# Optimization experiments

Measured on AMD Instinct MI355X. Metric: run time of the kernel, lower is better.

Reference implementation:

```python
import jax, jax.numpy as jnp
import numpy as np

N_SAMPLES = 32768; WINDOW = 512; STEP = 256; N_FRAMES = 128
N_COEFFS = 257; N_ATOMS = 32; MODEL_DIM = 128
DILATIONS = (1, 3, 9, 27, 81, 243, 1)


def _conv1d(x, w, b=None, dilation=1, padding=0):
    o = jax.lax.conv_general_dilated(x, w, (1,), [(padding, padding)],
                                     rhs_dilation=(dilation,),
                                     dimension_numbers=('NCH', 'OIH', 'NCH'))
    return o if b is None else o + b[None, :, None]


def _leaky(x):
    return jnp.where(x >= 0, x, 0.2 * x)


def _lin_stack(x, ws, bs, ow, ob):
    # LinearOutputStack: hidden linears with leaky relu, final linear
    for i in range(ws.shape[0]):
        x = _leaky(x @ ws[i].T + bs[i])
    return x @ ow.T + ob


def _conv_up(z, lw, lb, cw, cb, fw, fb_):
    x = (z @ lw.T + lb).reshape(-1, MODEL_DIM, 8)
    for i in range(cw.shape[0]):
        x = jnp.repeat(x, 2, axis=-1)
        x = _leaky(_conv1d(x, cw[i], cb[i], padding=1))
    return _conv1d(x, fw, fb_, padding=1)


def _lin_upsample(x, out_len):
    # F.upsample(mode='linear', align_corners=False)
    L = x.shape[-1]
    src = jnp.clip((jnp.arange(out_len) + 0.5) * (L / out_len) - 0.5, 0.0, L - 1)
    i0 = jnp.floor(src).astype(jnp.int32)
    i1 = jnp.minimum(i0 + 1, L - 1)
    t = (src - i0).astype(x.dtype)
    return x[..., i0] * (1 - t) + x[..., i1] * t


def _generate_event(envelope, transfer, impulse_tf, impulse_noise):
    # envelope [N,1,S], transfer [N,257,2,128], impulse_tf [N,257,2]
    tf = jax.lax.complex(transfer[:, :, 0, :], transfer[:, :, 1, :])  # [N,257,128]
    itf = jax.lax.complex(impulse_tf[..., 0], impulse_tf[..., 1])     # [N,257]
    spec = jnp.fft.rfft(impulse_noise, norm='ortho') * itf
    impulse = jnp.fft.irfft(spec, n=WINDOW, norm='ortho')             # [N,512]
    env = jnp.pad(envelope[:, 0, :], ((0, 0), (0, STEP)))             # pad last frame
    win_idx = (jnp.arange(N_FRAMES) * STEP)[:, None] + jnp.arange(WINDOW)  # [128,512]
    env_frames = env[:, win_idx]                                      # [N,128,512]
    ham = (0.54 - 0.46 * jnp.cos(2 * jnp.pi * jnp.arange(WINDOW) / WINDOW)).astype(envelope.dtype)

    def step(carry, inp):
        env_f, tf_f = inp                      # [N,512], [N,257]
        nxt = impulse * env_f + carry
        s = jnp.fft.rfft(nxt, norm='ortho') * tf_f
        out = jnp.fft.irfft(s, n=WINDOW, norm='ortho') * ham
        return out, out

    _, frames = jax.lax.scan(step, jnp.zeros_like(impulse),
                             (env_frames.transpose(1, 0, 2), tf.transpose(2, 0, 1)))
    frames = frames.transpose(1, 0, 2)         # [N,128,512]
    buf = jnp.zeros((frames.shape[0], N_FRAMES * STEP + STEP), frames.dtype)
    buf = buf.at[:, win_idx].add(frames)       # overlap-add, hop 256
    return buf[:, :N_SAMPLES]


def reference(x, fb_w,
              db_scale_w, db_scale_b, db_gate_w, db_gate_b,
              db_out_w, db_out_b, db_next_w, db_next_b,
              env_lin_w, env_lin_b, env_conv_w, env_conv_b, env_fin_w, env_fin_b,
              tf_lin_w, tf_lin_b, tf_conv_w, tf_conv_b, tf_fin_w, tf_fin_b,
              imp_w, imp_b, imp_out_w, imp_out_b,
              room_w, room_b, room_out_w, room_out_b,
              mix_w, mix_b, mix_out_w, mix_out_b,
              rooms, impulse_noise):
    B = x.shape[0]
    # FilterBank: conv over raw audio, same length
    n = jax.lax.conv_general_dilated(x, fb_w, (1,), [(256, 255)],
                                     dimension_numbers=('NCH', 'OIH', 'NCH'))  # [B,128,S]
    acc = jnp.zeros_like(n)
    for i, d in enumerate(DILATIONS):
        skip = n
        s = _conv1d(n, db_scale_w[i], db_scale_b[i], dilation=d, padding=d)
        g = _conv1d(n, db_gate_w[i], db_gate_b[i], dilation=d, padding=d)
        h = jnp.tanh(s) * jax.nn.sigmoid(g)
        acc = acc + jnp.einsum('oc,bct->bot', db_out_w[i], h) + db_out_b[i][None, :, None]
        n = jnp.einsum('oc,bct->bot', db_next_w[i], h) + db_next_b[i][None, :, None] + skip
    xf = acc                                                   # [B,128,S]
    norms = jnp.linalg.norm(xf, axis=1)                        # [B,S]
    values, indices = jax.lax.top_k(norms, N_ATOMS)            # [B,32]
    latents = jnp.take_along_axis(xf, indices[:, None, :], axis=2)  # [B,128,32]
    latents = latents.transpose(0, 2, 1).reshape(B * N_ATOMS, MODEL_DIM)
    # EventGenerator
    env = _conv_up(latents, env_lin_w, env_lin_b, env_conv_w, env_conv_b, env_fin_w, env_fin_b) ** 2
    env = _lin_upsample(env, N_SAMPLES)                        # [N,1,S]
    transfer = _conv_up(latents, tf_lin_w, tf_lin_b, tf_conv_w, tf_conv_b, tf_fin_w, tf_fin_b)
    transfer = transfer.reshape(-1, N_COEFFS, 2, N_FRAMES)
    impulse_tf = _lin_stack(latents, imp_w, imp_b, imp_out_w, imp_out_b).reshape(-1, N_COEFFS, 2)
    atoms = _generate_event(env, transfer, impulse_tf, impulse_noise).reshape(B, N_ATOMS, N_SAMPLES)
    # scatter-add atoms at topk offsets into 2*S buffer
    pos = indices[:, :, None] + jnp.arange(N_SAMPLES)[None, None, :]   # [B,32,S]
    weighted = atoms * values[:, :, None]

    def scat(pos_b, w_b):
        return jnp.zeros(2 * N_SAMPLES, w_b.dtype).at[pos_b.reshape(-1)].add(w_b.reshape(-1))

    final = jax.vmap(scat)(pos, weighted)[:, None, :N_SAMPLES]         # [B,1,S]
    # reverb mix
    agg = jnp.max(xf, axis=-1)                                         # [B,128]
    r = _lin_stack(agg, room_w, room_b, room_out_w, room_out_b)        # [B,n_rooms]
    m = _lin_stack(agg, mix_w, mix_b, mix_out_w, mix_out_b).reshape(-1, 1, 1)
    ir = jax.nn.softmax(r, axis=-1) @ rooms                            # [B,S]
    fs = jnp.fft.rfft(final[:, 0, :], n=2 * N_SAMPLES)
    irs = jnp.fft.rfft(ir, n=2 * N_SAMPLES)
    wet = jnp.fft.irfft(fs * irs, n=2 * N_SAMPLES)[:, None, :N_SAMPLES]
    return m * wet + final * (1 - m)


def setup_inputs() -> dict:
    key = jax.random.key(0)
    ks = iter(jax.random.split(key, 64))

    def w(*shape, s=0.05):
        return jax.random.normal(next(ks), shape, dtype=jnp.float32) * s

    return {
        'x': jax.random.normal(next(ks), (4, 1, N_SAMPLES), dtype=jnp.float32),
        'fb_w': w(128, 1, 512),
        'db_scale_w': w(7, 128, 128, 3), 'db_scale_b': w(7, 128),
        'db_gate_w': w(7, 128, 128, 3), 'db_gate_b': w(7, 128),
        'db_out_w': w(7, 128, 128), 'db_out_b': w(7, 128),
        'db_next_w': w(7, 128, 128), 'db_next_b': w(7, 128),
        'env_lin_w': w(1024, 128), 'env_lin_b': w(1024),
        'env_conv_w': w(4, 128, 128, 3), 'env_conv_b': w(4, 128),
        'env_fin_w': w(1, 128, 3), 'env_fin_b': w(1),
        'tf_lin_w': w(1024, 128), 'tf_lin_b': w(1024),
        'tf_conv_w': w(4, 128, 128, 3), 'tf_conv_b': w(4, 128),
        'tf_fin_w': w(514, 128, 3), 'tf_fin_b': w(514),
        'imp_w': w(3, 128, 128), 'imp_b': w(3, 128),
        'imp_out_w': w(514, 128), 'imp_out_b': w(514),
        'room_w': w(3, 128, 128), 'room_b': w(3, 128),
        'room_out_w': w(8, 128), 'room_out_b': w(8),
        'mix_w': w(3, 128, 128), 'mix_b': w(3, 128),
        'mix_out_w': w(1, 128), 'mix_out_b': w(1),
        'rooms': w(8, N_SAMPLES, s=0.1),
        'impulse_noise': jax.random.uniform(next(ks), (1, WINDOW), minval=-1.0, maxval=1.0, dtype=jnp.float32),
    }
```

## Files before the change

### kernel.cpp

```cpp
#include <hip/hip_runtime.h>
#include <math.h>

#define NS 32768

static __device__ __forceinline__ float leakyf(float x){ return x >= 0.f ? x : 0.2f*x; }

__global__ void k_wtrans(const float* __restrict__ ws, const float* __restrict__ wg, float* __restrict__ wT)
{
    int idx = blockIdx.x*256 + threadIdx.x;
    const int total = 7*2*3*128*128;
    if (idx >= total) return;
    int o  = idx & 127;
    int cc = (idx >> 7) & 127;
    int j  = (idx >> 14) % 3;
    int sg = (idx / 49152) & 1;
    int l  = idx / 98304;
    const float* src = sg ? wg : ws;
    wT[idx] = src[((l*128 + o)*128 + cc)*3 + j];
}

__global__ void k_wtrans2(const float* __restrict__ wo, const float* __restrict__ wn,
                          float* __restrict__ woT, float* __restrict__ wnT)
{
    int idx = blockIdx.x*256 + threadIdx.x;
    if (idx >= 7*128*128) return;
    int o = idx & 127;
    int c = (idx >> 7) & 127;
    int l = idx >> 14;
    woT[idx] = wo[(l*128 + o)*128 + c];
    wnT[idx] = wn[(l*128 + o)*128 + c];
}

__global__ void k_wtrans_up(const float* __restrict__ ecw, const float* __restrict__ tcw,
                            const float* __restrict__ tfw, float* __restrict__ wtu, float* __restrict__ wtf)
{
    int idx = blockIdx.x*256 + threadIdx.x;
    if (idx < 393216) {
        int o = idx & 127;
        int j = (idx >> 7) % 3;
        int c = (idx / 384) & 127;
        int ml = idx / 49152;
        const float* src = (ml < 4 ? ecw : tcw) + (ml & 3)*49152;
        wtu[idx] = src[(o*128 + c)*3 + j];
    }
    if (idx < 208896) {
        int ct = idx % 544;
        int j = (idx / 544) % 3;
        int c = idx / 1632;
        wtf[idx] = (ct < 514) ? tfw[(ct*128 + c)*3 + j] : 0.f;
    }
}

__global__ __launch_bounds__(512) void k_front(const float* __restrict__ x, const float* __restrict__ fbw,
                                               float* __restrict__ n0)
{
    int b = blockIdx.y;
    int t0 = blockIdx.x * 64;
    int tid = threadIdx.x;
    int t = tid & 63, og = tid >> 6;
    __shared__ float xs[576];
    __shared__ float4 wl[2048];
    for (int i = tid; i < 575; i += 512) {
        int p = t0 + i - 256;
        xs[i] = ((unsigned)p < NS) ? x[b*NS + p] : 0.f;
    }
    float s[16];
    #pragma unroll
    for (int i = 0; i < 16; ++i) s[i] = 0.f;
    for (int kc = 0; kc < 8; ++kc) {
        __syncthreads();
        for (int i = tid; i < 2048; i += 512) {
            int c = i >> 4, k4 = i & 15;
            wl[i] = *(const float4*)(fbw + c*512 + kc*64 + k4*4);
        }
        __syncthreads();
        for (int k4 = 0; k4 < 16; ++k4) {
            int base = t + kc*64 + k4*4;
            float xv0 = xs[base+0], xv1 = xs[base+1], xv2 = xs[base+2], xv3 = xs[base+3];
            #pragma unroll
            for (int i = 0; i < 16; ++i) {
                float4 w = wl[(og*16 + i)*16 + k4];
                s[i] += w.x*xv0 + w.y*xv1 + w.z*xv2 + w.w*xv3;
            }
        }
    }
    #pragma unroll
    for (int i = 0; i < 16; ++i)
        n0[(size_t)(b*128 + og*16 + i)*NS + t0 + t] = s[i];
}

__global__ __launch_bounds__(512) void k_layer(const float* __restrict__ nin, float* __restrict__ nout,
        float* __restrict__ acc, const float* __restrict__ wTl,
        const float* __restrict__ bs, const float* __restrict__ bg,
        const float* __restrict__ woTl, const float* __restrict__ bo,
        const float* __restrict__ wnTl, const float* __restrict__ bn,
        int d, int first)
{
    __shared__ float pool[20480];
    int b = blockIdx.y;
    int t0 = blockIdx.x * 128;
    int tid = threadIdx.x;
    int l = tid & 31, og = tid >> 5;
    int o0 = og * 8;
    int t4 = l * 4;
    const float* nb = nin + (size_t)b*128*NS;
    const float4* wq = (const float4*)wTl;

    int sci = tid >> 5;
    int st4 = (tid & 31) * 4;
    int wsgA = 0,              wccA = (tid >> 5) & 15,        wo4A = tid & 31;
    int wsgB = (tid+512) >> 9, wccB = ((tid+512) >> 5) & 15,  wo4B = (tid+512) & 31;

    float4 sreg, wr0, wr1;
    {
        int p = t0 + st4 - d;
        const float* bp = nb + (size_t)sci*NS;
        float v0 = ((unsigned)(p+0) < NS) ? bp[p+0] : 0.f;
        float v1 = ((unsigned)(p+1) < NS) ? bp[p+1] : 0.f;
        float v2 = ((unsigned)(p+2) < NS) ? bp[p+2] : 0.f;
        float v3 = ((unsigned)(p+3) < NS) ? bp[p+3] : 0.f;
        sreg = make_float4(v0,v1,v2,v3);
        wr0 = wq[((wsgA*3 + 0)*128 + wccA)*32 + wo4A];
        wr1 = wq[((wsgB*3 + 0)*128 + wccB)*32 + wo4B];
    }

    float sA[8], sB[8], sC[8], sD[8], gA[8], gB[8], gC[8], gD[8];
    #pragma unroll
    for (int i = 0; i < 8; ++i) {
        float bv = bs[o0+i], gv = bg[o0+i];
        sA[i]=bv; sB[i]=bv; sC[i]=bv; sD[i]=bv;
        gA[i]=gv; gB[i]=gv; gC[i]=gv; gD[i]=gv;
    }

    #pragma unroll 1
    for (int cnt = 0; cnt < 24; ++cnt) {
        int cur = cnt & 1;
        ((float4*)(pool + cur*2048))[tid] = sreg;
        {
            float4* wb = (float4*)(pool + 4096 + cur*4096);
            wb[tid] = wr0; wb[tid + 512] = wr1;
        }
        if (cnt < 23) {
            int nxt = cnt + 1;
            int jn = nxt >> 3, cbn = nxt & 7;
            int p = t0 + st4 + (jn-1)*d;
            const float* bp = nb + (size_t)(cbn*16 + sci)*NS;
            float v0 = ((unsigned)(p+0) < NS) ? bp[p+0] : 0.f;
            float v1 = ((unsigned)(p+1) < NS) ? bp[p+1] : 0.f;
            float v2 = ((unsigned)(p+2) < NS) ? bp[p+2] : 0.f;
            float v3 = ((unsigned)(p+3) < NS) ? bp[p+3] : 0.f;
            sreg = make_float4(v0,v1,v2,v3);
            wr0 = wq[((wsgA*3 + jn)*128 + cbn*16 + wccA)*32 + wo4A];
            wr1 = wq[((wsgB*3 + jn)*128 + cbn*16 + wccB)*32 + wo4B];
        }
        __syncthreads();
        const float* sb = pool + cur*2048;
        const float4* wS4 = (const float4*)(pool + 4096 + cur*4096);
        const float4* wG4 = wS4 + 512;
        for (int ccx = 0; ccx < 16; ++ccx) {
            float4 nv = *(const float4*)(sb + ccx*128 + t4);
            #pragma unroll
            for (int i4 = 0; i4 < 2; ++i4) {
                float4 wsv = wS4[ccx*32 + og*2 + i4];
                float4 wgv = wG4[ccx*32 + og*2 + i4];
                int ib = i4*4;
#define ST1(CMP, OO) \
                sA[OO] += nv.x*wsv.CMP; sB[OO] += nv.y*wsv.CMP; sC[OO] += nv.z*wsv.CMP; sD[OO] += nv.w*wsv.CMP; \
                gA[OO] += nv.x*wgv.CMP; gB[OO] += nv.y*wgv.CMP; gC[OO] += nv.z*wgv.CMP; gD[OO] += nv.w*wgv.CMP;
                ST1(x, ib+0) ST1(y, ib+1) ST1(z, ib+2) ST1(w, ib+3)
#undef ST1
            }
        }
    }

    __syncthreads();
    #pragma unroll
    for (int i = 0; i < 8; ++i) {
        float h0 = tanhf(sA[i]) * (1.f/(1.f + __expf(-gA[i])));
        float h1 = tanhf(sB[i]) * (1.f/(1.f + __expf(-gB[i])));
        float h2 = tanhf(sC[i]) * (1.f/(1.f + __expf(-gC[i])));
        float h3 = tanhf(sD[i]) * (1.f/(1.f + __expf(-gD[i])));
        *(float4*)(pool + (o0+i)*128 + t4) = make_float4(h0,h1,h2,h3);
    }

    int aarm = tid >> 8, arest = tid & 255;
    int accx = arest >> 5, ao4 = arest & 31;
    float4 w2r;
    {
        const float4* src = (const float4*)(aarm ? wnTl : woTl);
        w2r = src[(0*8 + accx)*32 + ao4];
    }

    float aA[8], aB[8], aC[8], aD[8], nA[8], nB[8], nC[8], nD[8];
    #pragma unroll
    for (int i = 0; i < 8; ++i) { aA[i]=0.f;aB[i]=0.f;aC[i]=0.f;aD[i]=0.f;nA[i]=0.f;nB[i]=0.f;nC[i]=0.f;nD[i]=0.f; }

    #pragma unroll 1
    for (int cb2 = 0; cb2 < 16; ++cb2) {
        int cur = cb2 & 1;
        ((float4*)(pool + 16384 + cur*2048))[tid] = w2r;
        if (cb2 < 15) {
            const float4* src = (const float4*)(aarm ? wnTl : woTl);
            w2r = src[((cb2+1)*8 + accx)*32 + ao4];
        }
        __syncthreads();
        const float4* w2S = (const float4*)(pool + 16384 + cur*2048);
        const float4* w2N = w2S + 256;
        for (int ccx = 0; ccx < 8; ++ccx) {
            float4 hv = *(const float4*)(pool + (cb2*8 + ccx)*128 + t4);
            #pragma unroll
            for (int i4 = 0; i4 < 2; ++i4) {
                float4 wov = w2S[ccx*32 + og*2 + i4];
                float4 wnv = w2N[ccx*32 + og*2 + i4];
                int ib = i4*4;
#define ST2(CMP, OO) \
                aA[OO] += hv.x*wov.CMP; aB[OO] += hv.y*wov.CMP; aC[OO] += hv.z*wov.CMP; aD[OO] += hv.w*wov.CMP; \
                nA[OO] += hv.x*wnv.CMP; nB[OO] += hv.y*wnv.CMP; nC[OO] += hv.z*wnv.CMP; nD[OO] += hv.w*wnv.CMP;
                ST2(x, ib+0) ST2(y, ib+1) ST2(z, ib+2) ST2(w, ib+3)
#undef ST2
            }
        }
    }

    #pragma unroll
    for (int i = 0; i < 8; ++i) {
        int o = o0 + i;
        float bov = bo[o], bnv = bn[o];
        size_t gi = (size_t)(b*128 + o)*NS + t0 + t4;
        float4 av = first ? make_float4(0.f,0.f,0.f,0.f) : *(const float4*)(acc + gi);
        float4 nf = *(const float4*)(nin + gi);
        *(float4*)(acc + gi)  = make_float4(av.x + aA[i] + bov, av.y + aB[i] + bov,
                                            av.z + aC[i] + bov, av.w + aD[i] + bov);
        *(float4*)(nout + gi) = make_float4(nA[i] + bnv + nf.x, nB[i] + bnv + nf.y,
                                            nC[i] + bnv + nf.z, nD[i] + bnv + nf.w);
    }
}

__global__ void k_norms(const float* __restrict__ xf, float* __restrict__ norms)
{
    int b = blockIdx.y;
    int t = blockIdx.x*256 + threadIdx.x;
    float a = 0.f;
    for (int c = 0; c < 128; ++c) {
        float v = xf[(size_t)(b*128 + c)*NS + t];
        a += v*v;
    }
    norms[b*NS + t] = a;
}

__global__ __launch_bounds__(1024) void k_topk(float* __restrict__ norms, float* __restrict__ topv, int* __restrict__ topi)
{
    int b = blockIdx.x;
    int tid = threadIdx.x;
    __shared__ float rv[1024];
    __shared__ int   ri[1024];
    for (int it = 0; it < 32; ++it) {
        float best = -2.f; int bi = 0;
        for (int k = tid; k < NS; k += 1024) {
            float v = norms[b*NS + k];
            if (v > best) { best = v; bi = k; }
        }
        rv[tid] = best; ri[tid] = bi;
        __syncthreads();
        for (int off = 512; off > 0; off >>= 1) {
            if (tid < off) {
                float ov = rv[tid+off]; int oi = ri[tid+off];
                if (ov > rv[tid] || (ov == rv[tid] && oi < ri[tid])) { rv[tid] = ov; ri[tid] = oi; }
            }
            __syncthreads();
        }
        if (tid == 0) {
            topv[b*32 + it] = sqrtf(rv[0]);
            topi[b*32 + it] = ri[0];
            norms[b*NS + ri[0]] = -1.f;
        }
        __syncthreads();
    }
}

__global__ void k_latents(const float* __restrict__ xf, const int* __restrict__ topi, float* __restrict__ lat)
{
    int ev = blockIdx.x; int c = threadIdx.x;
    int b = ev >> 5;
    int idx = topi[ev];
    lat[ev*128 + c] = xf[(size_t)(b*128 + c)*NS + idx];
}

__global__ void k_aggmax(const float* __restrict__ xf, float* __restrict__ agg)
{
    int rc = blockIdx.x;
    int tid = threadIdx.x;
    __shared__ float red[256];
    float m = -3.4e38f;
    const float* row = xf + (size_t)rc*NS;
    for (int t = tid; t < NS; t += 256) m = fmaxf(m, row[t]);
    red[tid] = m; __syncthreads();
    for (int off = 128; off > 0; off >>= 1) {
        if (tid < off) red[tid] = fmaxf(red[tid], red[tid+off]);
        __syncthreads();
    }
    if (tid == 0) agg[rc] = red[0];
}

template<int L2, int NPASS>
__device__ __forceinline__ void up_layerS(const float* __restrict__ wbase, const float* __restrict__ bias,
                                          const float* __restrict__ inb, float* __restrict__ outb,
                                          float* __restrict__ wst, int tid)
{
    constexpr int Lin = L2/2;
    constexpr int OGC = 512/L2;
    constexpr int OR  = 128/NPASS;
    constexpr int NO  = OR/OGC;
    constexpr int LOG = (L2==16)?4:(L2==32)?5:(L2==64)?6:7;
    int p  = tid & (L2-1);
    int og = tid >> LOG;
    int o0 = og*NO;
    #pragma unroll 1
    for (int pass = 0; pass < NPASS; ++pass) {
        int obase = pass*OR;
        float acc[NO];
        #pragma unroll
        for (int k = 0; k < NO; ++k) acc[k] = 0.f;
        #pragma unroll 1
        for (int cc0 = 0; cc0 < 128; cc0 += 16) {
            __syncthreads();
            for (int k = tid; k < 16*3*OR; k += 512) {
                int ci = k / (3*OR); int rem = k - ci*(3*OR);
                int j = rem / OR; int oo = rem - j*OR;
                wst[k] = wbase[(cc0+ci)*384 + j*128 + obase + oo];
            }
            __syncthreads();
            #pragma unroll 1
            for (int ci = 0; ci < 16; ++ci) {
                int c = cc0 + ci;
                float xv[3];
                #pragma unroll
                for (int j = 0; j < 3; ++j) {
                    int iu = p + j - 1;
                    xv[j] = ((unsigned)iu < (unsigned)L2) ? inb[c*Lin + (iu>>1)] : 0.f;
                }
                #pragma unroll
                for (int j = 0; j < 3; ++j) {
                    const float4* w4 = (const float4*)(wst + ci*3*OR + j*OR + o0);
                    #pragma unroll
                    for (int q = 0; q < NO/4; ++q) {
                        float4 w = w4[q];
                        acc[q*4+0] += xv[j]*w.x; acc[q*4+1] += xv[j]*w.y;
                        acc[q*4+2] += xv[j]*w.z; acc[q*4+3] += xv[j]*w.w;
                    }
                }
            }
        }
        #pragma unroll
        for (int k = 0; k < NO; ++k)
            outb[(obase + o0 + k)*L2 + p] = leakyf(acc[k] + bias[obase + o0 + k]);
    }
}

__global__ __launch_bounds__(512) void k_convup3(const float* __restrict__ lat,
    const float* __restrict__ elw, const float* __restrict__ elb, const float* __restrict__ ecb,
    const float* __restrict__ efw, const float* __restrict__ efb,
    const float* __restrict__ tlw, const float* __restrict__ tlb, const float* __restrict__ tcb,
    const float* __restrict__ tfb, const float* __restrict__ wtu, const float* __restrict__ wtf,
    float* __restrict__ envsq, float* __restrict__ tfT)
{
    __shared__ float pool[35008];
    float* latv = pool;
    float* bufA = pool + 128;
    float* bufB = pool + 4288;
    float* bufC = pool + 12480;
    float* wst  = pool + 28864;
    int ev = blockIdx.x;
    int m  = blockIdx.y;
    int tid = threadIdx.x;
    const float* lw = m ? tlw : elw;
    const float* lb = m ? tlb : elb;
    const float* cb = m ? tcb : ecb;
    const float* wu = wtu + m*4*49152;
    if (tid < 128) latv[tid] = lat[ev*128 + tid];
    __syncthreads();
    for (int jj = tid; jj < 1024; jj += 512) {
        float a = lb[jj];
        const float4* w4 = (const float4*)(lw + jj*128);
        #pragma unroll 8
        for (int q = 0; q < 32; ++q) {
            float4 w = w4[q];
            a += w.x*latv[q*4] + w.y*latv[q*4+1] + w.z*latv[q*4+2] + w.w*latv[q*4+3];
        }
        bufA[(jj>>3)*8 + (jj&7)] = a;
    }
    up_layerS<16,1>(wu,        cb,     bufA, bufB, wst, tid);
    up_layerS<32,1>(wu+49152,  cb+128, bufB, bufA, wst, tid);
    up_layerS<64,2>(wu+98304,  cb+256, bufA, bufB, wst, tid);
    up_layerS<128,4>(wu+147456,cb+384, bufB, bufC, wst, tid);
    __syncthreads();
    int p = tid & 127, g = tid >> 7;
    if (m == 0) {
        float s = 0.f;
        #pragma unroll 1
        for (int c = g*32; c < g*32+32; ++c) {
            #pragma unroll
            for (int j = 0; j < 3; ++j) {
                int iu = p + j - 1;
                float xv = ((unsigned)iu < 128u) ? bufC[c*128 + iu] : 0.f;
                s += efw[c*3+j]*xv;
            }
        }
        wst[g*128 + p] = s;
        __syncthreads();
        if (g == 0) {
            float a = wst[p] + wst[128+p] + wst[256+p] + wst[384+p] + efb[0];
            envsq[ev*128 + p] = a*a;
        }
    } else {
        float* trb = bufA;
        #pragma unroll 1
        for (int ctb = 0; ctb < 17; ++ctb) {
            int ct0 = ctb*32;
            float acc[8];
            #pragma unroll
            for (int i = 0; i < 8; ++i) acc[i] = 0.f;
            #pragma unroll 1
            for (int cc0 = 0; cc0 < 128; cc0 += 16) {
                __syncthreads();
                for (int k = tid; k < 1536; k += 512) {
                    int ci = k / 96, rem = k - ci*96;
                    int j = rem >> 5, ctl = rem & 31;
                    wst[k] = wtf[(cc0+ci)*1632 + j*544 + ct0 + ctl];
                }
                __syncthreads();
                #pragma unroll 1
                for (int ci = 0; ci < 16; ++ci) {
                    int c = cc0 + ci;
                    float xv[3];
                    #pragma unroll
                    for (int j = 0; j < 3; ++j) {
                        int iu = p + j - 1;
                        xv[j] = ((unsigned)iu < 128u) ? bufC[c*128 + iu] : 0.f;
                    }
                    #pragma unroll
                    for (int j = 0; j < 3; ++j) {
                        const float4* w4 = (const float4*)(wst + ci*96 + j*32 + g*8);
                        #pragma unroll
                        for (int q = 0; q < 2; ++q) {
                            float4 w = w4[q];
                            acc[q*4+0] += xv[j]*w.x; acc[q*4+1] += xv[j]*w.y;
                            acc[q*4+2] += xv[j]*w.z; acc[q*4+3] += xv[j]*w.w;
                        }
                    }
                }
            }
            __syncthreads();
            #pragma unroll
            for (int i = 0; i < 8; ++i) trb[(g*8 + i)*129 + p] = acc[i];
            __syncthreads();
            int ctl2 = tid & 31, pg = tid >> 5;
            #pragma unroll 1
            for (int ps = 0; ps < 8; ++ps) {
                int pp = ps*16 + pg;
                int ct = ct0 + ctl2;
                if (ct < 514)
                    tfT[(size_t)(ev*128 + pp)*514 + ct] = trb[ctl2*129 + pp] + tfb[ct];
            }
            __syncthreads();
        }
    }
}

__global__ __launch_bounds__(128) void k_itf(const float* __restrict__ lat,
    const float* __restrict__ iw, const float* __restrict__ ib,
    const float* __restrict__ iow, const float* __restrict__ iob,
    float* __restrict__ itf)
{
    int ev = blockIdx.x; int tid = threadIdx.x;
    __shared__ float xa[128], xb[128];
    xa[tid] = lat[ev*128 + tid];
    __syncthreads();
    float* src = xa; float* dst = xb;
    for (int l = 0; l < 3; ++l) {
        float a = ib[l*128 + tid];
        const float* wr = iw + (l*128 + tid)*128;
        for (int k = 0; k < 128; ++k) a += wr[k]*src[k];
        dst[tid] = leakyf(a);
        __syncthreads();
        float* tmp = src; src = dst; dst = tmp;
    }
    for (int o = tid; o < 514; o += 128) {
        float a = iob[o];
        const float* wr = iow + o*128;
        for (int k = 0; k < 128; ++k) a += wr[k]*src[k];
        itf[ev*514 + o] = a;
    }
}

__global__ __launch_bounds__(128) void k_roommix(const float* __restrict__ agg,
    const float* __restrict__ rw, const float* __restrict__ rb,
    const float* __restrict__ row_, const float* __restrict__ rob,
    const float* __restrict__ mw, const float* __restrict__ mb,
    const float* __restrict__ mow, const float* __restrict__ mob,
    float* __restrict__ probs, float* __restrict__ mval)
{
    int b = blockIdx.x; int tid = threadIdx.x;
    __shared__ float xa[128], xb[128], rr[8];
    xa[tid] = agg[b*128 + tid];
    __syncthreads();
    float* src = xa; float* dst = xb;
    for (int l = 0; l < 3; ++l) {
        float a = rb[l*128 + tid];
        const float* wr = rw + (l*128 + tid)*128;
        for (int k = 0; k < 128; ++k) a += wr[k]*src[k];
        dst[tid] = leakyf(a);
        __syncthreads();
        float* tmp = src; src = dst; dst = tmp;
    }
    if (tid < 8) {
        float a = rob[tid];
        const float* wr = row_ + tid*128;
        for (int k = 0; k < 128; ++k) a += wr[k]*src[k];
        rr[tid] = a;
    }
    __syncthreads();
    if (tid == 0) {
        float m = rr[0];
        for (int j = 1; j < 8; ++j) m = fmaxf(m, rr[j]);
        float ssum = 0.f; float e[8];
        for (int j = 0; j < 8; ++j) { e[j] = __expf(rr[j]-m); ssum += e[j]; }
        for (int j = 0; j < 8; ++j) probs[b*8+j] = e[j]/ssum;
    }
    __syncthreads();
    xa[tid] = agg[b*128 + tid];
    __syncthreads();
    src = xa; dst = xb;
    for (int l = 0; l < 3; ++l) {
        float a = mb[l*128 + tid];
        const float* wr = mw + (l*128 + tid)*128;
        for (int k = 0; k < 128; ++k) a += wr[k]*src[k];
        dst[tid] = leakyf(a);
        __syncthreads();
        float* tmp = src; src = dst; dst = tmp;
    }
    if (tid == 0) {
        float a = mob[0];
        for (int k = 0; k < 128; ++k) a += mow[k]*src[k];
        mval[b] = a;
    }
}

__global__ void k_ir(const float* __restrict__ probs, const float* __restrict__ rooms, float* __restrict__ ir)
{
    int b = blockIdx.y;
    int t = blockIdx.x*256 + threadIdx.x;
    float a = 0.f;
    for (int j = 0; j < 8; ++j) a += probs[b*8+j]*rooms[j*NS + t];
    ir[b*NS + t] = a;
}

__global__ void k_tfprep(const float* __restrict__ tfT, float2* __restrict__ Tscr)
{
    int f = blockIdx.x, ev = blockIdx.y;
    const float* tp = tfT + ((size_t)(ev*128 + f))*514;
    float2* dst = Tscr + ((size_t)(ev*128 + f))*512;
    int t = threadIdx.x;
    #pragma unroll
    for (int h = 0; h < 2; ++h) {
        int slot = t + h*256;
        int pos = (int)(__brev((unsigned)slot) >> 23);
        float2 H;
        if (pos == 0)        H = make_float2(tp[0], 0.f);
        else if (pos == 256) H = make_float2(tp[512], 0.f);
        else if (pos < 256)  H = make_float2(tp[2*pos], tp[2*pos+1]);
        else { int q = 512 - pos; H = make_float2(tp[2*q], -tp[2*q+1]); }
        dst[slot] = H;
    }
}

__global__ void k_itfprep(const float* __restrict__ itf, float2* __restrict__ iscr)
{
    int ev = blockIdx.x;
    const float* tp = itf + (size_t)ev*514;
    float2* dst = iscr + (size_t)ev*512;
    int t = threadIdx.x;
    #pragma unroll
    for (int h = 0; h < 2; ++h) {
        int slot = t + h*256;
        int pos = (int)(__brev((unsigned)slot) >> 23);
        float2 H;
        if (pos == 0)        H = make_float2(tp[0], 0.f);
        else if (pos == 256) H = make_float2(tp[512], 0.f);
        else if (pos < 256)  H = make_float2(tp[2*pos], tp[2*pos+1]);
        else { int q = 512 - pos; H = make_float2(tp[2*q], -tp[2*q+1]); }
        dst[slot] = H;
    }
}

__device__ __forceinline__ void fft_filt(float nx0, float nx1,
    const float2* __restrict__ Tf,
    float* __restrict__ re, float* __restrict__ im,
    const float* __restrict__ twr, const float* __restrict__ twi,
    int t, float& out0, float& out1)
{
    int w = t >> 6, l = t & 63;
    int c0 = (w << 7) + l;
    {
        float d = nx0 - nx1;
        re[t] = nx0 + nx1; im[t] = 0.f;
        re[t+256] = d * twr[t]; im[t+256] = d * twi[t];
    }
    __syncthreads();
    {
        int i = (t & 127) + ((t >> 7) << 8);
        int j = i & 127;
        float wr = twr[j*2], wi = twi[j*2];
        float ur = re[i], ui = im[i], vr = re[i+128], vi = im[i+128];
        re[i] = ur + vr; im[i] = ui + vi;
        float dr = ur - vr, di = ui - vi;
        re[i+128] = dr*wr - di*wi; im[i+128] = dr*wi + di*wr;
    }
    __syncthreads();
    float a0r = re[c0], a0i = im[c0], a1r = re[c0+64], a1i = im[c0+64];
    {
        float wr = twr[l*4], wi = twi[l*4];
        float ur = a0r, ui = a0i;
        a0r = ur + a1r; a0i = ui + a1i;
        float dr = ur - a1r, di = ui - a1i;
        a1r = dr*wr - di*wi; a1i = dr*wi + di*wr;
    }
#define DIFS(S, TS) { \
        int j = l & (S-1); float wr = twr[j*TS], wi = twi[j*TS]; \
        int up = l & S; \
        float o0r = __shfl_xor(a0r, S, 64), o0i = __shfl_xor(a0i, S, 64); \
        float o1r = __shfl_xor(a1r, S, 64), o1i = __shfl_xor(a1i, S, 64); \
        if (up) { float dr = o0r - a0r, di = o0i - a0i; a0r = dr*wr - di*wi; a0i = dr*wi + di*wr; \
                  float er = o1r - a1r, ei = o1i - a1i; a1r = er*wr - ei*wi; a1i = er*wi + ei*wr; } \
        else    { a0r += o0r; a0i += o0i; a1r += o1r; a1i += o1i; } }
    DIFS(32, 8) DIFS(16, 16) DIFS(8, 32) DIFS(4, 64) DIFS(2, 128) DIFS(1, 256)
#undef DIFS
    {
        float2 T0 = Tf[c0];
        float2 T1 = Tf[c0+64];
        float r = a0r*T0.x - a0i*T0.y; a0i = a0r*T0.y + a0i*T0.x; a0r = r;
        r = a1r*T1.x - a1i*T1.y; a1i = a1r*T1.y + a1i*T1.x; a1r = r;
    }
#define DITS(S, TS) { \
        int j = l & (S-1); float wr = twr[j*TS], wi = -twi[j*TS]; \
        int up = l & S; \
        if (up) { float r = a0r*wr - a0i*wi; a0i = a0r*wi + a0i*wr; a0r = r; \
                  r = a1r*wr - a1i*wi; a1i = a1r*wi + a1i*wr; a1r = r; } \
        float o0r = __shfl_xor(a0r, S, 64), o0i = __shfl_xor(a0i, S, 64); \
        float o1r = __shfl_xor(a1r, S, 64), o1i = __shfl_xor(a1i, S, 64); \
        if (up) { a0r = o0r - a0r; a0i = o0i - a0i; a1r = o1r - a1r; a1i = o1i - a1i; } \
        else    { a0r += o0r; a0i += o0i; a1r += o1r; a1i += o1i; } }
    DITS(1, 256) DITS(2, 128) DITS(4, 64) DITS(8, 32) DITS(16, 16) DITS(32, 8)
#undef DITS
    {
        float wr = twr[l*4], wi = -twi[l*4];
        float vr = a1r*wr - a1i*wi, vi = a1r*wi + a1i*wr;
        a1r = a0r - vr; a1i = a0i - vi;
        a0r += vr; a0i += vi;
    }
    __syncthreads();
    re[c0] = a0r; im[c0] = a0i; re[c0+64] = a1r; im[c0+64] = a1i;
    __syncthreads();
    {
        int i = (t & 127) + ((t >> 7) << 8);
        int j = i & 127;
        float wr = twr[j*2], wi = -twi[j*2];
        float ur = re[i], ui = im[i];
        float br = re[i+128], bi = im[i+128];
        float vr = br*wr - bi*wi, vi = br*wi + bi*wr;
        re[i] = ur + vr; im[i] = ui + vi;
        re[i+128] = ur - vr; im[i+128] = ui - vi;
    }
    __syncthreads();
    {
        float wr = twr[t], wi = -twi[t];
        float ur = re[t];
        float br = re[t+256], bi = im[t+256];
        float vr = br*wr - bi*wi;
        out0 = ur + vr;
        out1 = ur - vr;
    }
}

__global__ __launch_bounds__(256) void k_event(const float2* __restrict__ Tscr, const float2* __restrict__ itfscr,
    const float* __restrict__ envsq, const float* __restrict__ noise, float* __restrict__ atoms)
{
    int ev = blockIdx.x; int t = threadIdx.x;
    __shared__ float twr[256], twi[256], re[512], im[512], envl[128];
    if (t < 128) envl[t] = envsq[ev*128 + t];
    {
        float ang = -6.283185307179586f * (float)t / 512.0f;
        float si, co;
        sincosf(ang, &si, &co);
        twr[t] = co; twi[t] = si;
    }
    float ham0 = 0.54f - 0.46f*cosf(6.283185307179586f*(float)t/512.0f);
    float ham1 = 0.54f - 0.46f*cosf(6.283185307179586f*(float)(t+256)/512.0f);
    __syncthreads();
    float imp0, imp1;
    fft_filt(noise[t], noise[t+256], itfscr + (size_t)ev*512, re, im, twr, twi, t, imp0, imp1);
    const float inv512 = 1.f/512.f;
    imp0 *= inv512; imp1 *= inv512;
    float carry0 = 0.f, carry1 = 0.f, accv = 0.f;
    #pragma unroll 1
    for (int f = 0; f < 128; ++f) {
        float e0, e1;
        {
            int tg = f*256 + t;
            float srcp = ((float)tg + 0.5f)*(1.0f/256.0f) - 0.5f;
            srcp = fminf(fmaxf(srcp, 0.f), 127.f);
            int i0 = (int)srcp; float fr = srcp - (float)i0;
            int i1 = i0 + 1; if (i1 > 127) i1 = 127;
            e0 = envl[i0]*(1.f-fr) + envl[i1]*fr;
        }
        {
            int tg = f*256 + 256 + t;
            e1 = 0.f;
            if (tg < NS) {
                float srcp = ((float)tg + 0.5f)*(1.0f/256.0f) - 0.5f;
                srcp = fminf(fmaxf(srcp, 0.f), 127.f);
                int i0 = (int)srcp; float fr = srcp - (float)i0;
                int i1 = i0 + 1; if (i1 > 127) i1 = 127;
                e1 = envl[i0]*(1.f-fr) + envl[i1]*fr;
            }
        }
        float nx0 = imp0*e0 + carry0;
        float nx1 = imp1*e1 + carry1;
        float o0, o1;
        fft_filt(nx0, nx1, Tscr + ((size_t)(ev*128 + f))*512, re, im, twr, twi, t, o0, o1);
        o0 *= inv512 * ham0;
        o1 *= inv512 * ham1;
        atoms[(size_t)ev*NS + f*256 + t] = o0 + accv;
        accv = o1; carry0 = o0; carry1 = o1;
    }
}

__global__ void k_gather(const float* __restrict__ atoms, const float* __restrict__ topv,
                         const int* __restrict__ topi, float* __restrict__ fin)
{
    int b = blockIdx.y;
    int t = blockIdx.x*256 + threadIdx.x;
    float s = 0.f;
    for (int a = 0; a < 32; ++a) {
        int ii = topi[b*32 + a];
        if (ii <= t) s += topv[b*32 + a] * atoms[(size_t)(b*32 + a)*NS + (t - ii)];
    }
    fin[b*NS + t] = s;
}

__global__ __launch_bounds__(256) void k_wetpart(const float* __restrict__ fin, const float* __restrict__ ir,
                                                 float* __restrict__ wetp)
{
    int t0 = blockIdx.x*256;
    int by = blockIdx.y;
    int b = by >> 3, cg = by & 7;
    int tid = threadIdx.x;
    __shared__ float fs[256];
    __shared__ float irw[512];
    float wet = 0.f;
    int nch = t0/256 + 1;
    #pragma unroll 1
    for (int q = cg; q < nch; q += 8) {
        int c0 = q*256;
        __syncthreads();
        fs[tid] = fin[b*NS + c0 + tid];
        int dmin = t0 - c0 - 255;
        for (int qq = tid; qq < 511; qq += 256) {
            int dd = dmin + qq;
            irw[qq] = ((unsigned)dd < NS) ? ir[b*NS + dd] : 0.f;
        }
        __syncthreads();
        if (c0 < t0) {
            #pragma unroll 8
            for (int k = 0; k < 256; ++k) wet += fs[k]*irw[tid + 255 - k];
        } else {
            for (int k = 0; k <= tid; ++k) wet += fs[k]*irw[tid + 255 - k];
        }
    }
    wetp[(size_t)by*NS + t0 + tid] = wet;
}

__global__ __launch_bounds__(256) void k_wetsum(const float* __restrict__ fin, const float* __restrict__ wetp,
                                                const float* __restrict__ mval, float* __restrict__ out)
{
    int b = blockIdx.y;
    int t = blockIdx.x*256 + threadIdx.x;
    float w = 0.f;
    #pragma unroll
    for (int cg = 0; cg < 8; ++cg) w += wetp[(size_t)(b*8+cg)*NS + t];
    float m = mval[b];
    float fv = fin[b*NS + t];
    out[b*NS + t] = m*w + fv*(1.f - m);
}

extern "C" void kernel_launch(void* const* d_in, const int* in_sizes, int n_in,
                              void* d_out, int out_size, void* d_ws, size_t ws_size,
                              hipStream_t stream)
{
    (void)in_sizes; (void)n_in; (void)out_size; (void)ws_size;
    const float* x    = (const float*)d_in[0];
    const float* fbw  = (const float*)d_in[1];
    const float* dsw  = (const float*)d_in[2];
    const float* dsb  = (const float*)d_in[3];
    const float* dgw  = (const float*)d_in[4];
    const float* dgb  = (const float*)d_in[5];
    const float* dow  = (const float*)d_in[6];
    const float* dob  = (const float*)d_in[7];
    const float* dnw  = (const float*)d_in[8];
    const float* dnb  = (const float*)d_in[9];
    const float* elw  = (const float*)d_in[10];
    const float* elb  = (const float*)d_in[11];
    const float* ecw  = (const float*)d_in[12];
    const float* ecb  = (const float*)d_in[13];
    const float* efw  = (const float*)d_in[14];
    const float* efb  = (const float*)d_in[15];
    const float* tlw  = (const float*)d_in[16];
    const float* tlb  = (const float*)d_in[17];
    const float* tcw  = (const float*)d_in[18];
    const float* tcb  = (const float*)d_in[19];
    const float* tfw  = (const float*)d_in[20];
    const float* tfb  = (const float*)d_in[21];
    const float* iw   = (const float*)d_in[22];
    const float* ib   = (const float*)d_in[23];
    const float* iow  = (const float*)d_in[24];
    const float* iob  = (const float*)d_in[25];
    const float* rw   = (const float*)d_in[26];
    const float* rb   = (const float*)d_in[27];
    const float* row_ = (const float*)d_in[28];
    const float* rob  = (const float*)d_in[29];
    const float* mw   = (const float*)d_in[30];
    const float* mb   = (const float*)d_in[31];
    const float* mow  = (const float*)d_in[32];
    const float* mob  = (const float*)d_in[33];
    const float* rooms= (const float*)d_in[34];
    const float* noise= (const float*)d_in[35];

    float* ws   = (float*)d_ws;
    float* n0   = ws;
    float* n1   = ws + 16777216;
    float* accb = ws + 33554432;
    float* wT   = ws + 50331648;
    float* woT  = ws + 51707904;
    float* wnT  = ws + 51822592;
    float* envsq= ws + 51937280;
    float* lat  = ws + 51953664;
    float* itfb = ws + 51970048;
    float* norms= ws + 52035840;
    float* topv = ws + 52166912;
    int*   topi = (int*)(ws + 52167040);
    float* agg  = ws + 52167168;
    float* probs= ws + 52167680;
    float* mval = ws + 52167712;
    float* irb  = ws + 52167744;
    float* fin  = ws + 52298816;
    float* tfT  = n0;
    float* atoms= n0 + 8421376;
    float* wetp = n0 + 12615680;
    float* wtu  = n1;
    float* wtf  = n1 + 393216;
    float2* Tscr   = (float2*)n1;
    float2* itfscr = (float2*)accb;

    float* out = (float*)d_out;

    k_wtrans<<<dim3((1376256+255)/256), dim3(256), 0, stream>>>(dsw, dgw, wT);
    k_wtrans2<<<dim3((114688+255)/256), dim3(256), 0, stream>>>(dow, dnw, woT, wnT);
    k_front<<<dim3(512,4), dim3(512), 0, stream>>>(x, fbw, n0);

    const int dil[7] = {1,3,9,27,81,243,1};
    float* cin = n0; float* cout = n1;
    for (int l = 0; l < 7; ++l) {
        k_layer<<<dim3(256,4), dim3(512), 0, stream>>>(
            cin, cout, accb, wT + l*98304,
            dsb + l*128, dgb + l*128,
            woT + l*16384, dob + l*128,
            wnT + l*16384, dnb + l*128,
            dil[l], l==0 ? 1 : 0);
        float* tmp = cin; cin = cout; cout = tmp;
    }
    k_norms<<<dim3(128,4), dim3(256), 0, stream>>>(accb, norms);
    k_topk<<<dim3(4), dim3(1024), 0, stream>>>(norms, topv, topi);
    k_latents<<<dim3(128), dim3(128), 0, stream>>>(accb, topi, lat);
    k_aggmax<<<dim3(512), dim3(256), 0, stream>>>(accb, agg);
    k_wtrans_up<<<dim3(1536), dim3(256), 0, stream>>>(ecw, tcw, tfw, wtu, wtf);
    k_convup3<<<dim3(128,2), dim3(512), 0, stream>>>(lat, elw, elb, ecb, efw, efb,
                                                     tlw, tlb, tcb, tfb, wtu, wtf, envsq, tfT);
    k_itf<<<dim3(128), dim3(128), 0, stream>>>(lat, iw, ib, iow, iob, itfb);
    k_roommix<<<dim3(4), dim3(128), 0, stream>>>(agg, rw, rb, row_, rob, mw, mb, mow, mob, probs, mval);
    k_ir<<<dim3(128,4), dim3(256), 0, stream>>>(probs, rooms, irb);
    k_tfprep<<<dim3(128,128), dim3(256), 0, stream>>>(tfT, Tscr);
    k_itfprep<<<dim3(128), dim3(256), 0, stream>>>(itfb, itfscr);
    k_event<<<dim3(128), dim3(256), 0, stream>>>(Tscr, itfscr, envsq, noise, atoms);
    k_gather<<<dim3(128,4), dim3(256), 0, stream>>>(atoms, topv, topi, fin);
    k_wetpart<<<dim3(128,32), dim3(256), 0, stream>>>(fin, irb, wetp);
    k_wetsum<<<dim3(128,4), dim3(256), 0, stream>>>(fin, wetp, mval, out);
}
```

Baseline: 5.002 ms.

## Split transfer-function final conv into separate kernel parallelized over output channel blocks

The final 514-channel conv of the transfer-function upsampler used to run serially inside k_convup3, with one block per event looping over 17 output-channel tiles. That loop is now a new kernel, k_tffin, launched over a 17x128 grid, which spreads the work over many more blocks. The upsampled activations are written to global memory and reloaded into shared memory in the new kernel. The output layout becomes channel-major with the 128 frames contiguous, and k_tfprep changes its indexing to match. The cost is an extra launch, a global round trip of the activations, and strided reads in k_tfprep.

Measured after the change: 4.651 ms. 1.08x faster.

```diff
diff --git a/kernel.cpp b/kernel.cpp
--- a/kernel.cpp
+++ b/kernel.cpp
@@ -361,8 +361,8 @@
     const float* __restrict__ elw, const float* __restrict__ elb, const float* __restrict__ ecb,
     const float* __restrict__ efw, const float* __restrict__ efb,
     const float* __restrict__ tlw, const float* __restrict__ tlb, const float* __restrict__ tcb,
-    const float* __restrict__ tfb, const float* __restrict__ wtu, const float* __restrict__ wtf,
-    float* __restrict__ envsq, float* __restrict__ tfT)
+    const float* __restrict__ wtu,
+    float* __restrict__ envsq, float* __restrict__ Xg)
 {
     __shared__ float pool[35008];
     float* latv = pool;
@@ -394,8 +394,8 @@
     up_layerS<64,2>(wu+98304,  cb+256, bufA, bufB, wst, tid);
     up_layerS<128,4>(wu+147456,cb+384, bufB, bufC, wst, tid);
     __syncthreads();
-    int p = tid & 127, g = tid >> 7;
     if (m == 0) {
+        int p = tid & 127, g = tid >> 7;
         float s = 0.f;
         #pragma unroll 1
         for (int c = g*32; c < g*32+32; ++c) {
@@ -413,57 +413,61 @@
             envsq[ev*128 + p] = a*a;
         }
     } else {
-        float* trb = bufA;
+        float* xg = Xg + (size_t)ev*16384;
+        for (int k = tid*4; k < 16384; k += 2048)
+            *(float4*)(xg + k) = *(const float4*)(bufC + k);
+    }
+}
+
+__global__ __launch_bounds__(256) void k_tffin(const float* __restrict__ Xg, const float* __restrict__ wtf,
+                                               const float* __restrict__ tfb, float* __restrict__ tfTt)
+{
+    __shared__ float pool[17920];
+    float* Xs  = pool;
+    float* wst = pool + 16384;
+    int ctb = blockIdx.x, ev = blockIdx.y;
+    int ct0 = ctb*32;
+    int tid = threadIdx.x;
+    int p = tid & 127, g = tid >> 7;
+    const float* xg = Xg + (size_t)ev*16384;
+    for (int k = tid*4; k < 16384; k += 1024)
+        *(float4*)(Xs + k) = *(const float4*)(xg + k);
+    float acc[16];
+    #pragma unroll
+    for (int i = 0; i < 16; ++i) acc[i] = 0.f;
+    #pragma unroll 1
+    for (int cc0 = 0; cc0 < 128; cc0 += 16) {
+        __syncthreads();
+        for (int k = tid; k < 1536; k += 256) {
+            int ci = k / 96, rem = k - ci*96;
+            int j = rem >> 5, ctl = rem & 31;
+            wst[k] = wtf[(cc0+ci)*1632 + j*544 + ct0 + ctl];
+        }
+        __syncthreads();
         #pragma unroll 1
-        for (int ctb = 0; ctb < 17; ++ctb) {
-            int ct0 = ctb*32;
-            float acc[8];
+        for (int ci = 0; ci < 16; ++ci) {
+            const float* in = Xs + (cc0 + ci)*128;
+            float xm = (p >= 1)  ? in[p-1] : 0.f;
+            float x0 = in[p];
+            float xp = (p < 127) ? in[p+1] : 0.f;
             #pragma unroll
-            for (int i = 0; i < 8; ++i) acc[i] = 0.f;
-            #pragma unroll 1
-            for (int cc0 = 0; cc0 < 128; cc0 += 16) {
-                __syncthreads();
-                for (int k = tid; k < 1536; k += 512) {
-                    int ci = k / 96, rem = k - ci*96;
-                    int j = rem >> 5, ctl = rem & 31;
-                    wst[k] = wtf[(cc0+ci)*1632 + j*544 + ct0 + ctl];
-                }
-                __syncthreads();
-                #pragma unroll 1
-                for (int ci = 0; ci < 16; ++ci) {
-                    int c = cc0 + ci;
-                    float xv[3];
-                    #pragma unroll
-                    for (int j = 0; j < 3; ++j) {
-                        int iu = p + j - 1;
-                        xv[j] = ((unsigned)iu < 128u) ? bufC[c*128 + iu] : 0.f;
-                    }
-                    #pragma unroll
-                    for (int j = 0; j < 3; ++j) {
-                        const float4* w4 = (const float4*)(wst + ci*96 + j*32 + g*8);
-                        #pragma unroll
-                        for (int q = 0; q < 2; ++q) {
-                            float4 w = w4[q];
-                            acc[q*4+0] += xv[j]*w.x; acc[q*4+1] += xv[j]*w.y;
-                            acc[q*4+2] += xv[j]*w.z; acc[q*4+3] += xv[j]*w.w;
-                        }
-                    }
+            for (int j = 0; j < 3; ++j) {
+                float xv = (j == 0) ? xm : ((j == 1) ? x0 : xp);
+                const float4* w4 = (const float4*)(wst + ci*96 + j*32 + g*16);
+                #pragma unroll
+                for (int q = 0; q < 4; ++q) {
+                    float4 w = w4[q];
+                    acc[q*4+0] += xv*w.x; acc[q*4+1] += xv*w.y;
+                    acc[q*4+2] += xv*w.z; acc[q*4+3] += xv*w.w;
                 }
             }
-            __syncthreads();
-            #pragma unroll
-            for (int i = 0; i < 8; ++i) trb[(g*8 + i)*129 + p] = acc[i];
-            __syncthreads();
-            int ctl2 = tid & 31, pg = tid >> 5;
-            #pragma unroll 1
-            for (int ps = 0; ps < 8; ++ps) {
-                int pp = ps*16 + pg;
-                int ct = ct0 + ctl2;
-                if (ct < 514)
-                    tfT[(size_t)(ev*128 + pp)*514 + ct] = trb[ctl2*129 + pp] + tfb[ct];
-            }
-            __syncthreads();
-        }
+        }
+    }
+    #pragma unroll
+    for (int i = 0; i < 16; ++i) {
+        int ct = ct0 + g*16 + i;
+        float bias = (ct < 514) ? tfb[ct] : 0.f;
+        tfTt[((size_t)ev*544 + ct)*128 + p] = acc[i] + bias;
     }
 }
 
@@ -555,10 +559,10 @@
     ir[b*NS + t] = a;
 }
 
-__global__ void k_tfprep(const float* __restrict__ tfT, float2* __restrict__ Tscr)
+__global__ void k_tfprep(const float* __restrict__ tfTt, float2* __restrict__ Tscr)
 {
     int f = blockIdx.x, ev = blockIdx.y;
-    const float* tp = tfT + ((size_t)(ev*128 + f))*514;
+    const float* tp = tfTt + (size_t)ev*544*128;
     float2* dst = Tscr + ((size_t)(ev*128 + f))*512;
     int t = threadIdx.x;
     #pragma unroll
@@ -566,10 +570,10 @@
         int slot = t + h*256;
         int pos = (int)(__brev((unsigned)slot) >> 23);
         float2 H;
-        if (pos == 0)        H = make_float2(tp[0], 0.f);
-        else if (pos == 256) H = make_float2(tp[512], 0.f);
-        else if (pos < 256)  H = make_float2(tp[2*pos], tp[2*pos+1]);
-        else { int q = 512 - pos; H = make_float2(tp[2*q], -tp[2*q+1]); }
+        if (pos == 0)        H = make_float2(tp[0*128 + f], 0.f);
+        else if (pos == 256) H = make_float2(tp[512*128 + f], 0.f);
+        else if (pos < 256)  H = make_float2(tp[(2*pos)*128 + f], tp[(2*pos+1)*128 + f]);
+        else { int q = 512 - pos; H = make_float2(tp[(2*q)*128 + f], -tp[(2*q+1)*128 + f]); }
         dst[slot] = H;
     }
 }
@@ -853,9 +857,10 @@
     float* mval = ws + 52167712;
     float* irb  = ws + 52167744;
     float* fin  = ws + 52298816;
-    float* tfT  = n0;
-    float* atoms= n0 + 8421376;
-    float* wetp = n0 + 12615680;
+    float* tfTt = n0;
+    float* atoms= n0 + 8912896;
+    float* wetp = n0 + 13107200;
+    float* Xg   = n0 + 14155776;
     float* wtu  = n1;
     float* wtf  = n1 + 393216;
     float2* Tscr   = (float2*)n1;
@@ -884,11 +889,12 @@
     k_aggmax<<<dim3(512), dim3(256), 0, stream>>>(accb, agg);
     k_wtrans_up<<<dim3(1536), dim3(256), 0, stream>>>(ecw, tcw, tfw, wtu, wtf);
     k_convup3<<<dim3(128,2), dim3(512), 0, stream>>>(lat, elw, elb, ecb, efw, efb,
-                                                     tlw, tlb, tcb, tfb, wtu, wtf, envsq, tfT);
+                                                     tlw, tlb, tcb, wtu, envsq, Xg);
+    k_tffin<<<dim3(17,128), dim3(256), 0, stream>>>(Xg, wtf, tfb, tfTt);
     k_itf<<<dim3(128), dim3(128), 0, stream>>>(lat, iw, ib, iow, iob, itfb);
     k_roommix<<<dim3(4), dim3(128), 0, stream>>>(agg, rw, rb, row_, rob, mw, mb, mow, mob, probs, mval);
     k_ir<<<dim3(128,4), dim3(256), 0, stream>>>(probs, rooms, irb);
-    k_tfprep<<<dim3(128,128), dim3(256), 0, stream>>>(tfT, Tscr);
+    k_tfprep<<<dim3(128,128), dim3(256), 0, stream>>>(tfTt, Tscr);
     k_itfprep<<<dim3(128), dim3(256), 0, stream>>>(itfb, itfscr);
     k_event<<<dim3(128), dim3(256), 0, stream>>>(Tscr, itfscr, envsq, noise, atoms);
     k_gather<<<dim3(128,4), dim3(256), 0, stream>>>(atoms, topv, topi, fin);
```
